# Kernel optimization log

Measured on AMD Instinct MI355X. Metric: run time of the kernel, lower is better.

## Reference

```python
import jax, jax.numpy as jnp
import numpy as np

B, T, C = 2, 4096, 512
H = 8
D = C // H  # head_dim = 64


def setup_inputs() -> dict:
    key = jax.random.key(0)
    ks = jax.random.split(key, 9)
    s = 0.02
    return {
        "x": jax.random.normal(ks[0], (B, T, C), dtype=jnp.float32),
        "wq": jax.random.normal(ks[1], (C, C), dtype=jnp.float32) * s,
        "bq": jnp.zeros((C,), dtype=jnp.float32),
        "wk": jax.random.normal(ks[2], (C, C), dtype=jnp.float32) * s,
        "bk": jnp.zeros((C,), dtype=jnp.float32),
        "wv": jax.random.normal(ks[3], (C, C), dtype=jnp.float32) * s,
        "bv": jnp.zeros((C,), dtype=jnp.float32),
        "wo": jax.random.normal(ks[4], (C, C), dtype=jnp.float32) * s,
        "bo": jnp.zeros((C,), dtype=jnp.float32),
    }


def reference(x, wq, bq, wk, bk, wv, bv, wo, bo):
    Bx, Tx, Cx = x.shape
    # projections: y = x @ W^T + b (torch Linear convention: W is [out, in])
    q = (x @ wq.T + bq).reshape(Bx, Tx, H, D).transpose(0, 2, 1, 3)  # [B,H,T,D]
    k = (x @ wk.T + bk).reshape(Bx, Tx, H, D).transpose(0, 2, 1, 3)
    v = (x @ wv.T + bv).reshape(Bx, Tx, H, D).transpose(0, 2, 1, 3)
    scores = jnp.einsum("bhqd,bhkd->bhqk", q, k) * (D ** -0.5)  # [B,H,T,T]
    causal = jnp.tril(jnp.ones((Tx, Tx), dtype=bool))
    scores = jnp.where(causal, scores, -jnp.inf)
    weights = jax.nn.softmax(scores, axis=-1)
    o = jnp.einsum("bhqk,bhkd->bhqd", weights, v)  # [B,H,T,D]
    o = o.transpose(0, 2, 1, 3).reshape(Bx, Tx, Cx)
    return o @ wo.T + bo
```

## Files before the change

kernel.cpp:

```cpp
#include <hip/hip_runtime.h>
#include <math.h>

static constexpr int Bb = 2;
static constexpr int Tt = 4096;
static constexpr int Cc = 512;
static constexpr int Hh = 8;
static constexpr int Dd = 64;
static constexpr int Mtot = Bb * Tt;

#define QSCALE 0.1803368801111f
#define DEFER_THR 11.5f

typedef __attribute__((ext_vector_type(8)))  short   short8;
typedef __attribute__((ext_vector_type(4)))  float   f32x4;
typedef __attribute__((ext_vector_type(16))) float   f32x16;
typedef __attribute__((ext_vector_type(4)))  unsigned int   uint4v;
typedef __attribute__((ext_vector_type(4)))  unsigned short ushort4v;

__device__ inline unsigned short f2bf(float f) {
    unsigned int u = __float_as_uint(f);
    u += 0x7fffu + ((u >> 16) & 1u);
    return (unsigned short)(u >> 16);
}

__device__ inline unsigned int cvtpk_bf16(float a, float b) {
    unsigned int r;
    asm("v_cvt_pk_bf16_f32 %0, %1, %2" : "=v"(r) : "v"(a), "v"(b));
    return r;
}

__device__ inline int SW(int row) { return (row ^ (row >> 3)) & 7; }

__device__ inline void gload16(const void* g, void* lds) {
    __builtin_amdgcn_global_load_lds(
        (const __attribute__((address_space(1))) void*)g,
        (__attribute__((address_space(3))) void*)lds, 16, 0, 0);
}

__global__ __launch_bounds__(256)
void cast_f32_bf16(const float* __restrict__ src, unsigned short* __restrict__ dst) {
    const size_t i = ((size_t)blockIdx.x * 256 + threadIdx.x) * 8;
    const float4 a = *reinterpret_cast<const float4*>(src + i);
    const float4 b = *reinterpret_cast<const float4*>(src + i + 4);
    short8 o;
    o[0] = (short)f2bf(a.x); o[1] = (short)f2bf(a.y);
    o[2] = (short)f2bf(a.z); o[3] = (short)f2bf(a.w);
    o[4] = (short)f2bf(b.x); o[5] = (short)f2bf(b.y);
    o[6] = (short)f2bf(b.z); o[7] = (short)f2bf(b.w);
    *reinterpret_cast<short8*>(dst + i) = o;
}

__global__ __launch_bounds__(256)
void cast_w4(const float* __restrict__ w0, const float* __restrict__ w1,
             const float* __restrict__ w2, const float* __restrict__ w3,
             unsigned short* __restrict__ dst) {
    const float* srcs[4] = {w0, w1, w2, w3};
    const float* s = srcs[blockIdx.y];
    unsigned short* d = dst + (size_t)blockIdx.y * (Cc * Cc);
    const size_t i = ((size_t)blockIdx.x * 256 + threadIdx.x) * 8;
    const float4 a = *reinterpret_cast<const float4*>(s + i);
    const float4 b = *reinterpret_cast<const float4*>(s + i + 4);
    short8 o;
    o[0] = (short)f2bf(a.x); o[1] = (short)f2bf(a.y);
    o[2] = (short)f2bf(a.z); o[3] = (short)f2bf(a.w);
    o[4] = (short)f2bf(b.x); o[5] = (short)f2bf(b.y);
    o[6] = (short)f2bf(b.z); o[7] = (short)f2bf(b.w);
    *reinterpret_cast<short8*>(d + i) = o;
}

__global__ __launch_bounds__(256)
void proj_qkv(const unsigned short* __restrict__ A, const unsigned short* __restrict__ Wall,
              const float* __restrict__ bq, const float* __restrict__ bk,
              const float* __restrict__ bv,
              unsigned short* __restrict__ qo, unsigned short* __restrict__ ko,
              unsigned short* __restrict__ vo) {
    __shared__ unsigned short As[128][32];
    __shared__ unsigned short Bs[128][32];

    const int which = blockIdx.z;
    const unsigned short* Wb = Wall + (size_t)which * Cc * Cc;
    const float* bias = (which == 0) ? bq : (which == 1) ? bk : bv;
    unsigned short* outp = (which == 0) ? qo : (which == 1) ? ko : vo;
    const float scale = (which == 0) ? QSCALE : 1.0f;

    const int tid = threadIdx.x;
    const int lane = tid & 63;
    const int w = tid >> 6;
    const int wr = w >> 1, wc = w & 1;
    const int l15 = lane & 15, lg = lane >> 4;
    const int m0 = blockIdx.x * 128, n0 = blockIdx.y * 128;

    f32x4 acc[4][4] = {};

    for (int k0 = 0; k0 < Cc; k0 += 32) {
        #pragma unroll
        for (int i = 0; i < 2; ++i) {
            const int idx = tid + i * 256;
            const int row = idx >> 2, g = idx & 3;
            *reinterpret_cast<short8*>(&As[row][g * 8]) =
                *reinterpret_cast<const short8*>(&A[(size_t)(m0 + row) * Cc + k0 + g * 8]);
            *reinterpret_cast<short8*>(&Bs[row][g * 8]) =
                *reinterpret_cast<const short8*>(&Wb[(size_t)(n0 + row) * Cc + k0 + g * 8]);
        }
        __syncthreads();
        short8 a[4], b[4];
        #pragma unroll
        for (int mi = 0; mi < 4; ++mi)
            a[mi] = *reinterpret_cast<const short8*>(&As[wr * 64 + mi * 16 + l15][lg * 8]);
        #pragma unroll
        for (int nj = 0; nj < 4; ++nj)
            b[nj] = *reinterpret_cast<const short8*>(&Bs[wc * 64 + nj * 16 + l15][lg * 8]);
        #pragma unroll
        for (int mi = 0; mi < 4; ++mi)
            #pragma unroll
            for (int nj = 0; nj < 4; ++nj)
                acc[mi][nj] = __builtin_amdgcn_mfma_f32_16x16x32_bf16(a[mi], b[nj], acc[mi][nj], 0, 0, 0);
        __syncthreads();
    }

    #pragma unroll
    for (int mi = 0; mi < 4; ++mi) {
        #pragma unroll
        for (int nj = 0; nj < 4; ++nj) {
            const int col = n0 + wc * 64 + nj * 16 + l15;
            const float bvv = bias[col];
            if (which == 2) {
                const int mbase = m0 + wr * 64 + mi * 16 + lg * 4;
                const int b_ = mbase >> 12, t = mbase & (Tt - 1);
                const int h = col >> 6, d = col & 63;
                ushort4v o;
                #pragma unroll
                for (int r = 0; r < 4; ++r)
                    o[r] = f2bf(acc[mi][nj][r] + bvv);
                *reinterpret_cast<ushort4v*>(
                    &outp[(((size_t)b_ * Hh + h) * Dd + d) * Tt + t]) = o;
            } else {
                #pragma unroll
                for (int r = 0; r < 4; ++r) {
                    const int row = m0 + wr * 64 + mi * 16 + lg * 4 + r;
                    const int b_ = row >> 12, t = row & (Tt - 1);
                    const int h = col >> 6, d = col & 63;
                    outp[(((size_t)b_ * Hh + h) * Tt + t) * Dd + d] =
                        f2bf((acc[mi][nj][r] + bvv) * scale);
                }
            }
        }
    }
}

__global__ __launch_bounds__(256)
void proj_out(const unsigned short* __restrict__ A, const unsigned short* __restrict__ Wb,
              const float* __restrict__ bias, float* __restrict__ outp) {
    __shared__ unsigned short As[128][32];
    __shared__ unsigned short Bs[128][32];

    const int tid = threadIdx.x;
    const int lane = tid & 63;
    const int w = tid >> 6;
    const int wr = w >> 1, wc = w & 1;
    const int l15 = lane & 15, lg = lane >> 4;
    const int m0 = blockIdx.x * 128, n0 = blockIdx.y * 128;

    f32x4 acc[4][4] = {};

    for (int k0 = 0; k0 < Cc; k0 += 32) {
        #pragma unroll
        for (int i = 0; i < 2; ++i) {
            const int idx = tid + i * 256;
            const int row = idx >> 2, g = idx & 3;
            *reinterpret_cast<short8*>(&As[row][g * 8]) =
                *reinterpret_cast<const short8*>(&A[(size_t)(m0 + row) * Cc + k0 + g * 8]);
            *reinterpret_cast<short8*>(&Bs[row][g * 8]) =
                *reinterpret_cast<const short8*>(&Wb[(size_t)(n0 + row) * Cc + k0 + g * 8]);
        }
        __syncthreads();
        short8 a[4], b[4];
        #pragma unroll
        for (int mi = 0; mi < 4; ++mi)
            a[mi] = *reinterpret_cast<const short8*>(&As[wr * 64 + mi * 16 + l15][lg * 8]);
        #pragma unroll
        for (int nj = 0; nj < 4; ++nj)
            b[nj] = *reinterpret_cast<const short8*>(&Bs[wc * 64 + nj * 16 + l15][lg * 8]);
        #pragma unroll
        for (int mi = 0; mi < 4; ++mi)
            #pragma unroll
            for (int nj = 0; nj < 4; ++nj)
                acc[mi][nj] = __builtin_amdgcn_mfma_f32_16x16x32_bf16(a[mi], b[nj], acc[mi][nj], 0, 0, 0);
        __syncthreads();
    }

    #pragma unroll
    for (int mi = 0; mi < 4; ++mi) {
        #pragma unroll
        for (int nj = 0; nj < 4; ++nj) {
            const int col = n0 + wc * 64 + nj * 16 + l15;
            const float bv = bias[col];
            #pragma unroll
            for (int r = 0; r < 4; ++r) {
                const int row = m0 + wr * 64 + mi * 16 + lg * 4 + r;
                outp[(size_t)row * Cc + col] = acc[mi][nj][r] + bv;
            }
        }
    }
}

__global__ __launch_bounds__(256)
void attn_mfma(const unsigned short* __restrict__ qb, const unsigned short* __restrict__ kb,
               const unsigned short* __restrict__ vtb, unsigned short* __restrict__ ob) {
    __shared__ unsigned short Ks[3][64][64];
    __shared__ unsigned short Vts[3][64][64];
    __shared__ float stats[4][32];

    const int bid = (int)blockIdx.x;
    const int qt = (bid < 256) ? (31 - (bid >> 4)) : ((bid - 256) >> 4);
    const int bh = bid & 15;

    const int tid = threadIdx.x;
    const int w = tid >> 6;
    const int lane = tid & 63;
    const int l31 = lane & 31, hi = lane >> 5;

    const int qg = qt * 128 + w * 32 + l31;

    short8 qf[4];
    {
        const unsigned short* qp = qb + ((size_t)bh * Tt + qg) * Dd + hi * 8;
        #pragma unroll
        for (int s = 0; s < 4; ++s)
            qf[s] = *reinterpret_cast<const short8*>(qp + s * 16);
    }

    const unsigned short* kb_h = kb + (size_t)bh * Tt * Dd;
    const unsigned short* vt_h = vtb + (size_t)bh * Dd * Tt;
    const int r0 = (w << 4) + (lane >> 3);
    const int r1 = r0 + 8;
    const int gk0 = ((lane & 7) ^ SW(r0)) * 8;
    const int gk1 = ((lane & 7) ^ SW(r1)) * 8;

    f32x16 oacc[2] = {};
    float mrow = -INFINITY, lrow = 0.f;

    const int ntiles = 2 * qt + 2;
    const int qmax_w = qt * 128 + w * 32 + 31;

    #pragma unroll
    for (int t = 0; t < 2; ++t) {
        gload16(kb_h + (size_t)(t * 64 + r0) * Dd + gk0, &Ks[t][(w << 4)][0]);
        gload16(kb_h + (size_t)(t * 64 + r1) * Dd + gk1, &Ks[t][(w << 4) + 8][0]);
        gload16(vt_h + (size_t)r0 * Tt + t * 64 + gk0, &Vts[t][(w << 4)][0]);
        gload16(vt_h + (size_t)r1 * Tt + t * 64 + gk1, &Vts[t][(w << 4) + 8][0]);
    }

    int cur = 0;
    for (int kt = 0; kt < ntiles; ++kt) {
        if (kt + 1 < ntiles) {
            asm volatile("s_waitcnt vmcnt(4)" ::: "memory");
        } else {
            asm volatile("s_waitcnt vmcnt(0)" ::: "memory");
        }
        __builtin_amdgcn_s_barrier();
        __builtin_amdgcn_sched_barrier(0);

        if (kt + 2 < ntiles) {
            const int stg = (cur + 2 >= 3) ? (cur - 1) : (cur + 2);
            const int n64 = (kt + 2) * 64;
            gload16(kb_h + (size_t)(n64 + r0) * Dd + gk0, &Ks[stg][(w << 4)][0]);
            gload16(kb_h + (size_t)(n64 + r1) * Dd + gk1, &Ks[stg][(w << 4) + 8][0]);
            gload16(vt_h + (size_t)r0 * Tt + n64 + gk0, &Vts[stg][(w << 4)][0]);
            gload16(vt_h + (size_t)r1 * Tt + n64 + gk1, &Vts[stg][(w << 4) + 8][0]);
        }

        if (kt * 64 <= qmax_w) {
            f32x16 sacc[2];
            #pragma unroll
            for (int f = 0; f < 2; ++f) {
                f32x16 z = {};
                const int krow = f * 32 + l31;
                const int sw = SW(krow);
                #pragma unroll
                for (int s = 0; s < 4; ++s) {
                    const short8 kf = *reinterpret_cast<const short8*>(
                        &Ks[cur][krow][((2 * s + hi) ^ sw) * 8]);
                    z = __builtin_amdgcn_mfma_f32_32x32x16_bf16(kf, qf[s], z, 0, 0, 0);
                }
                sacc[f] = z;
            }

            if (kt * 64 + 63 > qt * 128 + w * 32) {
                #pragma unroll
                for (int f = 0; f < 2; ++f)
                    #pragma unroll
                    for (int r = 0; r < 16; ++r) {
                        const int kvg = kt * 64 + f * 32 + (r & 3) + 8 * (r >> 2) + 4 * hi;
                        if (kvg > qg) sacc[f][r] = -INFINITY;
                    }
            }

            float pmax = sacc[0][0];
            #pragma unroll
            for (int r = 1; r < 16; ++r) pmax = fmaxf(pmax, sacc[0][r]);
            #pragma unroll
            for (int r = 0; r < 16; ++r) pmax = fmaxf(pmax, sacc[1][r]);
            pmax = fmaxf(pmax, __shfl_xor(pmax, 32));

            if (__any(pmax > mrow + DEFER_THR)) {
                const float mnew = fmaxf(mrow, pmax);
                const float corr = exp2f(mrow - mnew);
                mrow = mnew;
                lrow *= corr;
                stats[w][l31] = corr;
                #pragma unroll
                for (int r = 0; r < 16; ++r) {
                    const float c = stats[w][(r & 3) + 8 * (r >> 2) + 4 * hi];
                    oacc[0][r] *= c;
                    oacc[1][r] *= c;
                }
            }

            float rs = 0.f;
            #pragma unroll
            for (int f = 0; f < 2; ++f)
                #pragma unroll
                for (int r = 0; r < 16; ++r) {
                    const float p = exp2f(sacc[f][r] - mrow);
                    sacc[f][r] = p;
                    rs += p;
                }
            lrow += rs;

            #pragma unroll
            for (int f = 0; f < 2; ++f) {
                #pragma unroll
                for (int s2 = 0; s2 < 2; ++s2) {
                    const int b0 = s2 * 8;
                    unsigned int c01 = cvtpk_bf16(sacc[f][b0 + 0], sacc[f][b0 + 1]);
                    unsigned int c23 = cvtpk_bf16(sacc[f][b0 + 2], sacc[f][b0 + 3]);
                    unsigned int c45 = cvtpk_bf16(sacc[f][b0 + 4], sacc[f][b0 + 5]);
                    unsigned int c67 = cvtpk_bf16(sacc[f][b0 + 6], sacc[f][b0 + 7]);
                    asm("v_permlane32_swap_b32 %0, %1" : "+v"(c01), "+v"(c45));
                    asm("v_permlane32_swap_b32 %0, %1" : "+v"(c23), "+v"(c67));
                    uint4v paw;
                    paw[0] = c01; paw[1] = c23; paw[2] = c45; paw[3] = c67;
                    const short8 pa = *reinterpret_cast<short8*>(&paw);
                    const int g = 4 * f + 2 * s2;
                    #pragma unroll
                    for (int nb = 0; nb < 2; ++nb) {
                        const int vrow = nb * 32 + l31;
                        const short8 vf = *reinterpret_cast<const short8*>(
                            &Vts[cur][vrow][((g + hi) ^ SW(vrow)) * 8]);
                        oacc[nb] = __builtin_amdgcn_mfma_f32_32x32x16_bf16(pa, vf, oacc[nb], 0, 0, 0);
                    }
                }
            }
        }

        cur = (cur == 2) ? 0 : cur + 1;
    }

    const float lf = lrow + __shfl_xor(lrow, 32);
    stats[w][l31] = 1.f / lf;
    const int b_ = bh >> 3, h = bh & 7;
    #pragma unroll
    for (int r = 0; r < 16; ++r) {
        const int qr = (r & 3) + 8 * (r >> 2) + 4 * hi;
        const float linv = stats[w][qr];
        const int tg = qt * 128 + w * 32 + qr;
        unsigned short* dst = ob + ((size_t)b_ * Tt + tg) * Cc + h * Dd + l31;
        dst[0]  = f2bf(oacc[0][r] * linv);
        dst[32] = f2bf(oacc[1][r] * linv);
    }
}

extern "C" void kernel_launch(void* const* d_in, const int* in_sizes, int n_in,
                              void* d_out, int out_size, void* d_ws, size_t ws_size,
                              hipStream_t stream) {
    const float* x  = (const float*)d_in[0];
    const float* wq = (const float*)d_in[1];
    const float* bq = (const float*)d_in[2];
    const float* wk = (const float*)d_in[3];
    const float* bk = (const float*)d_in[4];
    const float* wv = (const float*)d_in[5];
    const float* bv = (const float*)d_in[6];
    const float* wo = (const float*)d_in[7];
    const float* bo = (const float*)d_in[8];
    float* out = (float*)d_out;

    const size_t nTok = (size_t)Mtot * Cc;
    const size_t nW   = (size_t)Cc * Cc;

    unsigned short* xb    = (unsigned short*)d_ws;
    unsigned short* wqb   = xb + nTok;
    unsigned short* wob   = wqb + 3 * nW;
    unsigned short* qbuf  = wqb + 4 * nW;
    unsigned short* kbuf  = qbuf + nTok;
    unsigned short* vtbuf = kbuf + nTok;
    unsigned short* oattb = vtbuf + nTok;

    cast_f32_bf16<<<dim3((unsigned)(nTok / 8 / 256)), 256, 0, stream>>>(x, xb);
    cast_w4<<<dim3((unsigned)(nW / 8 / 256), 4), 256, 0, stream>>>(wq, wk, wv, wo, wqb);

    proj_qkv<<<dim3(Mtot / 128, Cc / 128, 3), 256, 0, stream>>>(
        xb, wqb, bq, bk, bv, qbuf, kbuf, vtbuf);

    attn_mfma<<<dim3(512), 256, 0, stream>>>(qbuf, kbuf, vtbuf, oattb);

    proj_out<<<dim3(Mtot / 128, Cc / 128), 256, 0, stream>>>(oattb, wob, bo, out);
}
```

Measured before the change: 164.3 us.

## Split causal attention KV range into two halves with a separate combine kernel

Each query tile's KV loop is split into two blocks (1024 blocks total), each writing unnormalized fp32 partial outputs plus running max and sum to workspace. A new combine kernel merges the two halves with log-sum-exp rescaling and writes the bf16 attention output. This targets load imbalance and low occupancy from causal masking on a 512-block grid. The K/V pipeline also drops from triple to double buffering with a full vmcnt(0) wait, and the row-max reduction becomes a tree. The cost is an extra launch and fp32 partial-output traffic.

```diff
diff --git a/kernel.cpp b/kernel.cpp
--- a/kernel.cpp
+++ b/kernel.cpp
@@ -206,14 +206,20 @@
 
 __global__ __launch_bounds__(256)
 void attn_mfma(const unsigned short* __restrict__ qb, const unsigned short* __restrict__ kb,
-               const unsigned short* __restrict__ vtb, unsigned short* __restrict__ ob) {
-    __shared__ unsigned short Ks[3][64][64];
-    __shared__ unsigned short Vts[3][64][64];
+               const unsigned short* __restrict__ vtb,
+               float* __restrict__ opart, float2* __restrict__ mlp) {
+    __shared__ unsigned short Ks[2][64][64];
+    __shared__ unsigned short Vts[2][64][64];
     __shared__ float stats[4][32];
 
     const int bid = (int)blockIdx.x;
-    const int qt = (bid < 256) ? (31 - (bid >> 4)) : ((bid - 256) >> 4);
-    const int bh = bid & 15;
+    const int half = bid >> 9;
+    const int idx = bid & 511;
+    const int qt = half ? (idx >> 4) : (31 - (idx >> 4));
+    const int s  = half;
+    const int bh = idx & 15;
+    const int t0 = s ? (qt + 1) : 0;
+    const int t1 = s ? (2 * qt + 2) : (qt + 1);
 
     const int tid = threadIdx.x;
     const int w = tid >> 6;
@@ -226,8 +232,8 @@
     {
         const unsigned short* qp = qb + ((size_t)bh * Tt + qg) * Dd + hi * 8;
         #pragma unroll
-        for (int s = 0; s < 4; ++s)
-            qf[s] = *reinterpret_cast<const short8*>(qp + s * 16);
+        for (int sl = 0; sl < 4; ++sl)
+            qf[sl] = *reinterpret_cast<const short8*>(qp + sl * 16);
     }
 
     const unsigned short* kb_h = kb + (size_t)bh * Tt * Dd;
@@ -237,38 +243,30 @@
     const int gk0 = ((lane & 7) ^ SW(r0)) * 8;
     const int gk1 = ((lane & 7) ^ SW(r1)) * 8;
 
+    auto STAGE = [&](int t) {
+        const int n64 = t * 64;
+        const int bufi = t & 1;
+        gload16(kb_h + (size_t)(n64 + r0) * Dd + gk0, &Ks[bufi][(w << 4)][0]);
+        gload16(kb_h + (size_t)(n64 + r1) * Dd + gk1, &Ks[bufi][(w << 4) + 8][0]);
+        gload16(vt_h + (size_t)r0 * Tt + n64 + gk0, &Vts[bufi][(w << 4)][0]);
+        gload16(vt_h + (size_t)r1 * Tt + n64 + gk1, &Vts[bufi][(w << 4) + 8][0]);
+    };
+
     f32x16 oacc[2] = {};
     float mrow = -INFINITY, lrow = 0.f;
 
-    const int ntiles = 2 * qt + 2;
     const int qmax_w = qt * 128 + w * 32 + 31;
-
-    #pragma unroll
-    for (int t = 0; t < 2; ++t) {
-        gload16(kb_h + (size_t)(t * 64 + r0) * Dd + gk0, &Ks[t][(w << 4)][0]);
-        gload16(kb_h + (size_t)(t * 64 + r1) * Dd + gk1, &Ks[t][(w << 4) + 8][0]);
-        gload16(vt_h + (size_t)r0 * Tt + t * 64 + gk0, &Vts[t][(w << 4)][0]);
-        gload16(vt_h + (size_t)r1 * Tt + t * 64 + gk1, &Vts[t][(w << 4) + 8][0]);
-    }
-
-    int cur = 0;
-    for (int kt = 0; kt < ntiles; ++kt) {
-        if (kt + 1 < ntiles) {
-            asm volatile("s_waitcnt vmcnt(4)" ::: "memory");
-        } else {
-            asm volatile("s_waitcnt vmcnt(0)" ::: "memory");
-        }
+    const int qmin_w = qt * 128 + w * 32;
+
+    STAGE(t0);
+
+    for (int kt = t0; kt < t1; ++kt) {
+        const int cur = kt & 1;
+        asm volatile("s_waitcnt vmcnt(0)" ::: "memory");
         __builtin_amdgcn_s_barrier();
         __builtin_amdgcn_sched_barrier(0);
 
-        if (kt + 2 < ntiles) {
-            const int stg = (cur + 2 >= 3) ? (cur - 1) : (cur + 2);
-            const int n64 = (kt + 2) * 64;
-            gload16(kb_h + (size_t)(n64 + r0) * Dd + gk0, &Ks[stg][(w << 4)][0]);
-            gload16(kb_h + (size_t)(n64 + r1) * Dd + gk1, &Ks[stg][(w << 4) + 8][0]);
-            gload16(vt_h + (size_t)r0 * Tt + n64 + gk0, &Vts[stg][(w << 4)][0]);
-            gload16(vt_h + (size_t)r1 * Tt + n64 + gk1, &Vts[stg][(w << 4) + 8][0]);
-        }
+        if (kt + 1 < t1) STAGE(kt + 1);
 
         if (kt * 64 <= qmax_w) {
             f32x16 sacc[2];
@@ -278,15 +276,15 @@
                 const int krow = f * 32 + l31;
                 const int sw = SW(krow);
                 #pragma unroll
-                for (int s = 0; s < 4; ++s) {
+                for (int sl = 0; sl < 4; ++sl) {
                     const short8 kf = *reinterpret_cast<const short8*>(
-                        &Ks[cur][krow][((2 * s + hi) ^ sw) * 8]);
-                    z = __builtin_amdgcn_mfma_f32_32x32x16_bf16(kf, qf[s], z, 0, 0, 0);
+                        &Ks[cur][krow][((2 * sl + hi) ^ sw) * 8]);
+                    z = __builtin_amdgcn_mfma_f32_32x32x16_bf16(kf, qf[sl], z, 0, 0, 0);
                 }
                 sacc[f] = z;
             }
 
-            if (kt * 64 + 63 > qt * 128 + w * 32) {
+            if (kt * 64 + 63 > qmin_w) {
                 #pragma unroll
                 for (int f = 0; f < 2; ++f)
                     #pragma unroll
@@ -296,12 +294,15 @@
                     }
             }
 
-            float pmax = sacc[0][0];
-            #pragma unroll
-            for (int r = 1; r < 16; ++r) pmax = fmaxf(pmax, sacc[0][r]);
-            #pragma unroll
-            for (int r = 0; r < 16; ++r) pmax = fmaxf(pmax, sacc[1][r]);
-            pmax = fmaxf(pmax, __shfl_xor(pmax, 32));
+            float tr[16];
+            #pragma unroll
+            for (int r = 0; r < 16; ++r) tr[r] = fmaxf(sacc[0][r], sacc[1][r]);
+            #pragma unroll
+            for (int st = 8; st >= 1; st >>= 1)
+                #pragma unroll
+                for (int r = 0; r < 8; ++r)
+                    if (r < st) tr[r] = fmaxf(tr[r], tr[r + st]);
+            float pmax = fmaxf(tr[0], __shfl_xor(tr[0], 32));
 
             if (__any(pmax > mrow + DEFER_THR)) {
                 const float mnew = fmaxf(mrow, pmax);
@@ -353,22 +354,47 @@
                 }
             }
         }
-
-        cur = (cur == 2) ? 0 : cur + 1;
     }
 
     const float lf = lrow + __shfl_xor(lrow, 32);
-    stats[w][l31] = 1.f / lf;
-    const int b_ = bh >> 3, h = bh & 7;
+    const size_t pbase = ((size_t)s * 16 + bh) * Tt;
+    if (hi == 0) mlp[pbase + qg] = make_float2(mrow, lf);
     #pragma unroll
     for (int r = 0; r < 16; ++r) {
         const int qr = (r & 3) + 8 * (r >> 2) + 4 * hi;
-        const float linv = stats[w][qr];
         const int tg = qt * 128 + w * 32 + qr;
-        unsigned short* dst = ob + ((size_t)b_ * Tt + tg) * Cc + h * Dd + l31;
-        dst[0]  = f2bf(oacc[0][r] * linv);
-        dst[32] = f2bf(oacc[1][r] * linv);
-    }
+        float* dst = opart + (pbase + tg) * 64 + l31;
+        dst[0]  = oacc[0][r];
+        dst[32] = oacc[1][r];
+    }
+}
+
+__global__ __launch_bounds__(256)
+void combine(const float* __restrict__ opart, const float2* __restrict__ mlp,
+             unsigned short* __restrict__ ob) {
+    const int tid = threadIdx.x;
+    const int row = (int)blockIdx.x * 16 + (tid >> 4);
+    const int c4 = (tid & 15) * 4;
+    const size_t halfRows = (size_t)16 * Tt;
+
+    const float2 ml0 = mlp[row];
+    const float2 ml1 = mlp[halfRows + row];
+    const float m = fmaxf(ml0.x, ml1.x);
+    const float s0 = exp2f(ml0.x - m), s1 = exp2f(ml1.x - m);
+    const float inv = 1.f / (ml0.y * s0 + ml1.y * s1);
+
+    const float4 o0 = *reinterpret_cast<const float4*>(&opart[(size_t)row * 64 + c4]);
+    const float4 o1 = *reinterpret_cast<const float4*>(&opart[(halfRows + row) * 64 + c4]);
+
+    ushort4v o;
+    o[0] = f2bf((o0.x * s0 + o1.x * s1) * inv);
+    o[1] = f2bf((o0.y * s0 + o1.y * s1) * inv);
+    o[2] = f2bf((o0.z * s0 + o1.z * s1) * inv);
+    o[3] = f2bf((o0.w * s0 + o1.w * s1) * inv);
+
+    const int bh = row >> 12, t = row & (Tt - 1);
+    const int b_ = bh >> 3, h = bh & 7;
+    *reinterpret_cast<ushort4v*>(&ob[((size_t)b_ * Tt + t) * Cc + h * Dd + c4]) = o;
 }
 
 extern "C" void kernel_launch(void* const* d_in, const int* in_sizes, int n_in,
@@ -395,6 +421,8 @@
     unsigned short* kbuf  = qbuf + nTok;
     unsigned short* vtbuf = kbuf + nTok;
     unsigned short* oattb = vtbuf + nTok;
+    float*  opart = (float*)(oattb + nTok);
+    float2* mlp   = (float2*)(opart + (size_t)2 * 16 * Tt * 64);
 
     cast_f32_bf16<<<dim3((unsigned)(nTok / 8 / 256)), 256, 0, stream>>>(x, xb);
     cast_w4<<<dim3((unsigned)(nW / 8 / 256), 4), 256, 0, stream>>>(wq, wk, wv, wo, wqb);
@@ -402,7 +430,9 @@
     proj_qkv<<<dim3(Mtot / 128, Cc / 128, 3), 256, 0, stream>>>(
         xb, wqb, bq, bk, bv, qbuf, kbuf, vtbuf);
 
-    attn_mfma<<<dim3(512), 256, 0, stream>>>(qbuf, kbuf, vtbuf, oattb);
+    attn_mfma<<<dim3(1024), 256, 0, stream>>>(qbuf, kbuf, vtbuf, opart, mlp);
+
+    combine<<<dim3(16 * Tt / 16), 256, 0, stream>>>(opart, mlp, oattb);
 
     proj_out<<<dim3(Mtot / 128, Cc / 128), 256, 0, stream>>>(oattb, wob, bo, out);
 }
```

After: 170.0 us. 3.4% more time.
